# Optimization experiments

Measured on AMD Instinct MI355X. Metric: run time of the kernel, lower is better.

Reference implementation:

```python
import jax, jax.numpy as jnp
import numpy as np

NUM_HEADS = 6
HEAD_SIZE = 64
N_EMBD = 384


def setup_inputs() -> dict:
    key = jax.random.key(0)
    k1, k2, k3 = jax.random.split(key, 3)
    B, T, C = 256, 256, N_EMBD
    x = jax.random.normal(k1, (B, T, C), dtype=jnp.float32)
    # torch Linear(n_embd, 3*n_embd, bias=False): y = x @ W.T; store transposed for x @ W
    W_qkv = jax.random.normal(k2, (C, 3 * C), dtype=jnp.float32) * (1.0 / np.sqrt(C))
    W_proj = jax.random.normal(k3, (C, C), dtype=jnp.float32) * (1.0 / np.sqrt(C))
    b_proj = jnp.zeros((C,), dtype=jnp.float32)
    return {"x": x, "W_qkv": W_qkv, "W_proj": W_proj, "b_proj": b_proj}


def reference(x, W_qkv, W_proj, b_proj):
    B, T, C = x.shape
    H, D = NUM_HEADS, HEAD_SIZE
    qkv = x @ W_qkv                                  # [B, T, 3C]
    q, k, v = jnp.split(qkv, 3, axis=-1)
    # [B, T, C] -> [B, H, T, D]
    q = q.reshape(B, T, H, D).transpose(0, 2, 1, 3)
    k = k.reshape(B, T, H, D).transpose(0, 2, 1, 3)
    v = v.reshape(B, T, H, D).transpose(0, 2, 1, 3)
    att = jnp.einsum("bhtd,bhsd->bhts", q, k) / np.sqrt(D).astype(jnp.float32)
    causal = jnp.tril(jnp.ones((T, T), dtype=bool))  # tril buffer
    att = jnp.where(causal[None, None], att, -jnp.inf)
    att = jax.nn.softmax(att, axis=-1)
    # dropout layers are identity in eval mode
    out = jnp.einsum("bhts,bhsd->bhtd", att, v)      # [B, H, T, D]
    out = out.transpose(0, 2, 1, 3).reshape(B, T, C)
    return out @ W_proj.T @ jnp.eye(C, dtype=out.dtype) if False else out @ W_proj + b_proj
```

## Files before the change

### kernel.cpp

```cpp
#include <hip/hip_runtime.h>
#include <hip/hip_bf16.h>
#include <stdint.h>

typedef __hip_bfloat16 bf16;
using f32x4 = __attribute__((ext_vector_type(4))) float;
using s16x8 = __attribute__((ext_vector_type(8))) short;

#define MFMA16(A_, B_, C_) __builtin_amdgcn_mfma_f32_16x16x32_bf16((A_), (B_), (C_), 0, 0, 0)

__device__ __forceinline__ void gload16(const void* g, void* l) {
  __builtin_amdgcn_global_load_lds((const __attribute__((address_space(1))) void*)g,
                                   (__attribute__((address_space(3))) void*)l, 16, 0, 0);
}

__global__ __launch_bounds__(256) void detect_kernel(const void* __restrict__ x,
                                                     int* __restrict__ flag) {
  __shared__ int cnt;
  if (threadIdx.x == 0) cnt = 0;
  __syncthreads();
  const uint32_t* w = (const uint32_t*)x;
  int local = 0;
#pragma unroll
  for (int i = 0; i < 8; ++i) {
    uint32_t v = w[threadIdx.x * 8 + i];
    uint32_t e = (v >> 7) & 0xFF;
    if (e >= 110 && e <= 135) local++;
  }
  atomicAdd(&cnt, local);
  __syncthreads();
  if (threadIdx.x == 0) *flag = (cnt < 1024) ? 1 : 0;
}

__global__ __launch_bounds__(256) void convert_kernel(const void* __restrict__ x,
                                                      bf16* __restrict__ xb,
                                                      size_t elem_off,
                                                      const int* __restrict__ flag) {
  size_t i = ((size_t)blockIdx.x * 256 + threadIdx.x) * 8;
  if (*flag) {
    const float* xf = (const float*)x + elem_off + i;
    float4 a = ((const float4*)xf)[0];
    float4 b = ((const float4*)xf)[1];
    union { bf16 h[8]; uint4 u; } o;
    o.h[0] = __float2bfloat16(a.x); o.h[1] = __float2bfloat16(a.y);
    o.h[2] = __float2bfloat16(a.z); o.h[3] = __float2bfloat16(a.w);
    o.h[4] = __float2bfloat16(b.x); o.h[5] = __float2bfloat16(b.y);
    o.h[6] = __float2bfloat16(b.z); o.h[7] = __float2bfloat16(b.w);
    *(uint4*)(&xb[i]) = o.u;
  } else {
    *(uint4*)(&xb[i]) = *(const uint4*)((const bf16*)x + elem_off + i);
  }
}

__global__ __launch_bounds__(256) void transpose_kernel(const void* __restrict__ W,
                                                        bf16* __restrict__ Wt,
                                                        int K, int N,
                                                        const int* __restrict__ flag) {
  int idx = blockIdx.x * 256 + threadIdx.x;
  if (idx >= K * N) return;
  int n = idx / K;
  int k = idx - n * K;
  if (*flag)
    Wt[idx] = __float2bfloat16(((const float*)W)[k * N + n]);
  else
    Wt[idx] = ((const bf16*)W)[k * N + n];
}

template <int MODE>
__global__ __launch_bounds__(256) void gemm_kernel(
    const bf16* __restrict__ A, const bf16* __restrict__ Bt,
    bf16* __restrict__ qb, bf16* __restrict__ kb, bf16* __restrict__ vb,
    void* __restrict__ outp, const void* __restrict__ bias,
    int r_off, const int* __restrict__ flag) {
  constexpr int K = 384;
  __shared__ bf16 Ash[2][128 * 32];
  __shared__ bf16 Bsh[2][128 * 32];
  const int tid = threadIdx.x;
  const int lane = tid & 63;
  const int wave = tid >> 6;
  const int wm = wave & 1, wn = wave >> 1;
  const int l15 = lane & 15, quad = lane >> 4;

  const int nlin = gridDim.x * gridDim.y;
  const int orig = blockIdx.y * gridDim.x + blockIdx.x;
  const int xcd = orig & 7;
  const int q8 = nlin >> 3, r8 = nlin & 7;
  const int lin = (xcd < r8 ? xcd * (q8 + 1) : r8 * (q8 + 1) + (xcd - r8) * q8) + (orig >> 3);
  const int bx = lin % gridDim.x;
  const int by = lin / gridDim.x;
  const int n0 = bx * 128, m0 = by * 128;

  const int rl = lane >> 2;
  const int slot = lane & 3;
  const int sc = (slot - (lane >> 3)) & 3;
  const size_t lane_goff = (size_t)rl * K + sc * 8;

  const int arow0 = wave * 32;
  const bf16* Ag0 = A + (size_t)(m0 + arow0) * K + lane_goff;
  const bf16* Ag1 = Ag0 + (size_t)16 * K;
  const bf16* Bg0 = Bt + (size_t)(n0 + arow0) * K + lane_goff;
  const bf16* Bg1 = Bg0 + (size_t)16 * K;

  const int fc = ((quad + (l15 >> 1)) & 3) * 8;

  const f32x4 z4 = {0.f, 0.f, 0.f, 0.f};
  f32x4 acc[4][4];
#pragma unroll
  for (int i = 0; i < 4; ++i)
#pragma unroll
    for (int j = 0; j < 4; ++j) acc[i][j] = z4;

  auto stage = [&](int buf, int k0) {
    gload16(Ag0 + k0, &Ash[buf][arow0 * 32]);
    gload16(Ag1 + k0, &Ash[buf][(arow0 + 16) * 32]);
    gload16(Bg0 + k0, &Bsh[buf][arow0 * 32]);
    gload16(Bg1 + k0, &Bsh[buf][(arow0 + 16) * 32]);
  };

  stage(0, 0);
  __syncthreads();
  int cur = 0;
  for (int kt = 0; kt < 12; ++kt) {
    if (kt < 11) stage(cur ^ 1, (kt + 1) * 32);
    s16x8 af[4], bfr[4];
#pragma unroll
    for (int i = 0; i < 4; ++i) {
      af[i] = *(const s16x8*)(&Ash[cur][(wm * 64 + i * 16 + l15) * 32 + fc]);
      bfr[i] = *(const s16x8*)(&Bsh[cur][(wn * 64 + i * 16 + l15) * 32 + fc]);
    }
#pragma unroll
    for (int i = 0; i < 4; ++i)
#pragma unroll
      for (int j = 0; j < 4; ++j) acc[i][j] = MFMA16(af[i], bfr[j], acc[i][j]);
    __syncthreads();
    cur ^= 1;
  }

  const int mbase = m0 + wm * 64;
  const int nbase = n0 + wn * 64;
  if (MODE == 0) {
    const int sel = bx / 3;
    bf16* dst = (sel == 0) ? qb : ((sel == 1) ? kb : vb);
#pragma unroll
    for (int i = 0; i < 4; ++i) {
#pragma unroll
      for (int j = 0; j < 4; ++j) {
        int n_g = nbase + j * 16 + l15;
        int c = n_g - sel * 384;
        int h = c >> 6, d = c & 63;
#pragma unroll
        for (int r = 0; r < 4; ++r) {
          int m_loc = mbase + i * 16 + quad * 4 + r;
          int b = m_loc >> 8, t = m_loc & 255;
          bf16 bv = __float2bfloat16(acc[i][j][r]);
          int bh = b * 6 + h;
          if (sel < 2) {
            dst[(size_t)bh * 16384 + t * 64 + d] = bv;
          } else {
            int rr = t & 31;
            int pos = (((rr & 15) >> 2) << 3) | (rr & 3) | ((rr >> 4) << 2);
            int tt = (t & ~31) | pos;
            dst[(size_t)bh * 16384 + d * 256 + tt] = bv;
          }
        }
      }
    }
  } else {
    const int f32io = *flag;
#pragma unroll
    for (int i = 0; i < 4; ++i) {
#pragma unroll
      for (int j = 0; j < 4; ++j) {
        int n_g = nbase + j * 16 + l15;
        float bsv = f32io ? ((const float*)bias)[n_g]
                          : __bfloat162float(((const bf16*)bias)[n_g]);
#pragma unroll
        for (int r = 0; r < 4; ++r) {
          int m_loc = mbase + i * 16 + quad * 4 + r;
          size_t o = (size_t)(r_off + m_loc) * 384 + n_g;
          float val = acc[i][j][r] + bsv;
          if (f32io)
            ((float*)outp)[o] = val;
          else
            ((bf16*)outp)[o] = __float2bfloat16(val);
        }
      }
    }
  }
}

__global__ __launch_bounds__(256, 3) void attn_kernel(const bf16* __restrict__ Q,
                                                      const bf16* __restrict__ Kb,
                                                      const bf16* __restrict__ Vt,
                                                      bf16* __restrict__ attn_out) {
  const int tid = threadIdx.x;
  const int lane = tid & 63;
  const int wave = tid >> 6;
  const int l15 = lane & 15, quad = lane >> 4;
  const int nblk = gridDim.x;
  int blk = blockIdx.x;
  if ((nblk & 7) == 0)
    blk = (blockIdx.x & 7) * (nblk >> 3) + (blockIdx.x >> 3);
  const int p = blk & 1;
  const int bh = blk >> 1;
  const int jA = p * 4 + wave;
  const int jB = 15 - jA;
  const size_t base = (size_t)bh * 16384;
  const int q0A = jA * 16, q0B = jB * 16;

  s16x8 qA0 = *(const s16x8*)(&Q[base + (q0A + l15) * 64 + quad * 8]);
  s16x8 qA1 = *(const s16x8*)(&Q[base + (q0A + l15) * 64 + 32 + quad * 8]);
  s16x8 qB0 = *(const s16x8*)(&Q[base + (q0B + l15) * 64 + quad * 8]);
  s16x8 qB1 = *(const s16x8*)(&Q[base + (q0B + l15) * 64 + 32 + quad * 8]);

  const int ktA = (jA + 2) >> 1;
  const int ktB = (jB + 2) >> 1;
  const int tqA = q0A + l15, tqB = q0B + l15;
  const f32x4 z4 = {0.f, 0.f, 0.f, 0.f};

  const bf16* Kp = Kb + base + (size_t)l15 * 64 + quad * 8;
  const bf16* Vp = Vt + base + (size_t)l15 * 256 + quad * 8;

  typedef union { s16x8 v; uint32_t w[4]; } pf_t;

  s16x8 kf[3][4];
  s16x8 vf[2][4];
#pragma unroll
  for (int i = 0; i < 4; ++i) {
    kf[0][i] = *(const s16x8*)(Kp + (size_t)((i >> 1) * 16) * 64 + (i & 1) * 32);
    kf[1][i] = *(const s16x8*)(Kp + (size_t)(32 + (i >> 1) * 16) * 64 + (i & 1) * 32);
  }
#pragma unroll
  for (int dt = 0; dt < 4; ++dt) vf[0][dt] = *(const s16x8*)(Vp + (size_t)dt * 4096);

  f32x4 ofA[4], ofB[4];
#pragma unroll
  for (int dt = 0; dt < 4; ++dt) { ofA[dt] = z4; ofB[dt] = z4; }
  float rsA = 0.f, rsB = 0.f;

#pragma unroll
  for (int t = 0; t < 8; ++t) {
    if (t < ktB) {
      if (t + 2 < ktB) {
        const bf16* Kn = Kp + (size_t)(t + 2) * 32 * 64;
#pragma unroll
        for (int i = 0; i < 4; ++i)
          kf[(t + 2) % 3][i] = *(const s16x8*)(Kn + (size_t)((i >> 1) * 16) * 64 + (i & 1) * 32);
      }
      if (t + 1 < ktB) {
#pragma unroll
        for (int dt = 0; dt < 4; ++dt)
          vf[(t + 1) & 1][dt] = *(const s16x8*)(Vp + (size_t)dt * 4096 + (t + 1) * 32);
      }
      pf_t pfB;
#pragma unroll
      for (int hf = 0; hf < 2; ++hf) {
        const int nt = 2 * t + hf;
        if (nt <= jB) {
          f32x4 s = MFMA16(kf[t % 3][hf * 2 + 0], qB0, z4);
          s = MFMA16(kf[t % 3][hf * 2 + 1], qB1, s);
          const int tk0 = nt * 16 + quad * 4;
          float p0 = (tk0 + 0 <= tqB) ? __expf(s[0] * 0.125f) : 0.f;
          float p1 = (tk0 + 1 <= tqB) ? __expf(s[1] * 0.125f) : 0.f;
          float p2 = (tk0 + 2 <= tqB) ? __expf(s[2] * 0.125f) : 0.f;
          float p3 = (tk0 + 3 <= tqB) ? __expf(s[3] * 0.125f) : 0.f;
          rsB += (p0 + p1) + (p2 + p3);
          union { bf16 hh[2]; uint32_t u; } w0, w1;
          w0.hh[0] = __float2bfloat16(p0); w0.hh[1] = __float2bfloat16(p1);
          w1.hh[0] = __float2bfloat16(p2); w1.hh[1] = __float2bfloat16(p3);
          pfB.w[hf * 2 + 0] = w0.u;
          pfB.w[hf * 2 + 1] = w1.u;
        } else {
          pfB.w[hf * 2 + 0] = 0u;
          pfB.w[hf * 2 + 1] = 0u;
        }
      }
      if (t < ktA) {
        pf_t pfA;
#pragma unroll
        for (int hf = 0; hf < 2; ++hf) {
          const int nt = 2 * t + hf;
          if (nt <= jA) {
            f32x4 s = MFMA16(kf[t % 3][hf * 2 + 0], qA0, z4);
            s = MFMA16(kf[t % 3][hf * 2 + 1], qA1, s);
            const int tk0 = nt * 16 + quad * 4;
            float p0 = (tk0 + 0 <= tqA) ? __expf(s[0] * 0.125f) : 0.f;
            float p1 = (tk0 + 1 <= tqA) ? __expf(s[1] * 0.125f) : 0.f;
            float p2 = (tk0 + 2 <= tqA) ? __expf(s[2] * 0.125f) : 0.f;
            float p3 = (tk0 + 3 <= tqA) ? __expf(s[3] * 0.125f) : 0.f;
            rsA += (p0 + p1) + (p2 + p3);
            union { bf16 hh[2]; uint32_t u; } w0, w1;
            w0.hh[0] = __float2bfloat16(p0); w0.hh[1] = __float2bfloat16(p1);
            w1.hh[0] = __float2bfloat16(p2); w1.hh[1] = __float2bfloat16(p3);
            pfA.w[hf * 2 + 0] = w0.u;
            pfA.w[hf * 2 + 1] = w1.u;
          } else {
            pfA.w[hf * 2 + 0] = 0u;
            pfA.w[hf * 2 + 1] = 0u;
          }
        }
#pragma unroll
        for (int dt = 0; dt < 4; ++dt) ofA[dt] = MFMA16(vf[t & 1][dt], pfA.v, ofA[dt]);
      }
#pragma unroll
      for (int dt = 0; dt < 4; ++dt) ofB[dt] = MFMA16(vf[t & 1][dt], pfB.v, ofB[dt]);
    }
  }

  rsA += __shfl_xor(rsA, 16);
  rsA += __shfl_xor(rsA, 32);
  rsB += __shfl_xor(rsB, 16);
  rsB += __shfl_xor(rsB, 32);
  const float invA = 1.0f / rsA;
  const float invB = 1.0f / rsB;

  const int b = bh / 6;
  const int h = bh - b * 6;
  const size_t orowA = (size_t)(b * 256 + q0A + l15) * 384 + h * 64;
  const size_t orowB = (size_t)(b * 256 + q0B + l15) * 384 + h * 64;
#pragma unroll
  for (int dt = 0; dt < 4; ++dt) {
    union { bf16 h4[4]; uint2 u; } oa, ob;
#pragma unroll
    for (int r = 0; r < 4; ++r) {
      oa.h4[r] = __float2bfloat16(ofA[dt][r] * invA);
      ob.h4[r] = __float2bfloat16(ofB[dt][r] * invB);
    }
    *(uint2*)(&attn_out[orowA + dt * 16 + quad * 4]) = oa.u;
    *(uint2*)(&attn_out[orowB + dt * 16 + quad * 4]) = ob.u;
  }
}

extern "C" void kernel_launch(void* const* d_in, const int* in_sizes, int n_in,
                              void* d_out, int out_size, void* d_ws, size_t ws_size,
                              hipStream_t stream) {
  const void* x = d_in[0];
  const void* Wqkv = d_in[1];
  const void* Wproj = d_in[2];
  const void* bproj = d_in[3];

  char* ws = (char*)d_ws;
  int* flag = (int*)ws;                ws += 256;
  bf16* Wt_qkv = (bf16*)ws;            ws += (size_t)1152 * 384 * 2;
  bf16* Wt_proj = (bf16*)ws;           ws += (size_t)384 * 384 * 2;

  const size_t per_batch = (size_t)5 * 98304 * 2;
  size_t used = (size_t)(ws - (char*)d_ws);
  size_t remain = (ws_size > used) ? (ws_size - used) : 0;
  int NB = (int)(remain / per_batch);
  if (NB > 256) NB = 256;
  if (NB < 1) NB = 1;

  bf16* xb_buf = (bf16*)ws;
  bf16* q_buf = xb_buf + (size_t)NB * 98304;
  bf16* k_buf = q_buf + (size_t)NB * 98304;
  bf16* vt_buf = k_buf + (size_t)NB * 98304;
  bf16* attn_buf = vt_buf + (size_t)NB * 98304;

  detect_kernel<<<1, 256, 0, stream>>>(x, flag);
  transpose_kernel<<<(384 * 1152 + 255) / 256, 256, 0, stream>>>(Wqkv, Wt_qkv, 384, 1152, flag);
  transpose_kernel<<<(384 * 384 + 255) / 256, 256, 0, stream>>>(Wproj, Wt_proj, 384, 384, flag);

  for (int b0 = 0; b0 < 256; b0 += NB) {
    int nb = (256 - b0 < NB) ? (256 - b0) : NB;
    int r_off = b0 * 256;
    convert_kernel<<<nb * 48, 256, 0, stream>>>(x, xb_buf, (size_t)r_off * 384, flag);
    gemm_kernel<0><<<dim3(9, 2 * nb), 256, 0, stream>>>(
        xb_buf, Wt_qkv, q_buf, k_buf, vt_buf, nullptr, nullptr, 0, flag);
    attn_kernel<<<nb * 12, 256, 0, stream>>>(q_buf, k_buf, vt_buf, attn_buf);
    gemm_kernel<1><<<dim3(3, 2 * nb), 256, 0, stream>>>(
        attn_buf, Wt_proj, nullptr, nullptr, nullptr, d_out, bproj, r_off, flag);
  }
}
```

Measured before the change: 436.8 us.

## Enlarge GEMM tile to 256x128 with each wave owning 64 rows

The GEMM block tile grows from 128x128 to 256x128. Each of the four waves now computes a 64x128 slice, with 4x8 MFMA accumulators, and reads all eight B fragments from LDS. The goal is to cut LDS and global traffic per FLOP, since B fragments are shared across a wave's row tiles, and to halve the grid. The cost is more accumulator registers (launch bounds set to 2 waves per SIMD), twice the LDS for A, and fewer blocks, which may hurt occupancy and load balance.

```diff
diff --git a/kernel.cpp b/kernel.cpp
--- a/kernel.cpp
+++ b/kernel.cpp
@@ -66,18 +66,17 @@
 }
 
 template <int MODE>
-__global__ __launch_bounds__(256) void gemm_kernel(
+__global__ __launch_bounds__(256, 2) void gemm_kernel(
     const bf16* __restrict__ A, const bf16* __restrict__ Bt,
     bf16* __restrict__ qb, bf16* __restrict__ kb, bf16* __restrict__ vb,
     void* __restrict__ outp, const void* __restrict__ bias,
     int r_off, const int* __restrict__ flag) {
   constexpr int K = 384;
-  __shared__ bf16 Ash[2][128 * 32];
+  __shared__ bf16 Ash[2][256 * 32];
   __shared__ bf16 Bsh[2][128 * 32];
   const int tid = threadIdx.x;
   const int lane = tid & 63;
   const int wave = tid >> 6;
-  const int wm = wave & 1, wn = wave >> 1;
   const int l15 = lane & 15, quad = lane >> 4;
 
   const int nlin = gridDim.x * gridDim.y;
@@ -87,69 +86,65 @@
   const int lin = (xcd < r8 ? xcd * (q8 + 1) : r8 * (q8 + 1) + (xcd - r8) * q8) + (orig >> 3);
   const int bx = lin % gridDim.x;
   const int by = lin / gridDim.x;
-  const int n0 = bx * 128, m0 = by * 128;
+  const int n0 = bx * 128, m0 = by * 256;
 
   const int rl = lane >> 2;
   const int slot = lane & 3;
   const int sc = (slot - (lane >> 3)) & 3;
-  const size_t lane_goff = (size_t)rl * K + sc * 8;
-
-  const int arow0 = wave * 32;
-  const bf16* Ag0 = A + (size_t)(m0 + arow0) * K + lane_goff;
-  const bf16* Ag1 = Ag0 + (size_t)16 * K;
-  const bf16* Bg0 = Bt + (size_t)(n0 + arow0) * K + lane_goff;
-  const bf16* Bg1 = Bg0 + (size_t)16 * K;
+
+  const bf16* Ag = A + (size_t)(m0 + wave * 16 + rl) * K + sc * 8;
+  const bf16* Bg = Bt + (size_t)(n0 + wave * 16 + rl) * K + sc * 8;
+
+  auto stage = [&](int buf, int k0) {
+#pragma unroll
+    for (int qd = 0; qd < 4; ++qd)
+      gload16(Ag + (size_t)qd * 64 * K + k0, &Ash[buf][(qd * 64 + wave * 16) * 32]);
+#pragma unroll
+    for (int h = 0; h < 2; ++h)
+      gload16(Bg + (size_t)h * 64 * K + k0, &Bsh[buf][(h * 64 + wave * 16) * 32]);
+  };
 
   const int fc = ((quad + (l15 >> 1)) & 3) * 8;
-
   const f32x4 z4 = {0.f, 0.f, 0.f, 0.f};
-  f32x4 acc[4][4];
+  f32x4 acc[4][8];
 #pragma unroll
   for (int i = 0; i < 4; ++i)
 #pragma unroll
-    for (int j = 0; j < 4; ++j) acc[i][j] = z4;
-
-  auto stage = [&](int buf, int k0) {
-    gload16(Ag0 + k0, &Ash[buf][arow0 * 32]);
-    gload16(Ag1 + k0, &Ash[buf][(arow0 + 16) * 32]);
-    gload16(Bg0 + k0, &Bsh[buf][arow0 * 32]);
-    gload16(Bg1 + k0, &Bsh[buf][(arow0 + 16) * 32]);
-  };
+    for (int j = 0; j < 8; ++j) acc[i][j] = z4;
 
   stage(0, 0);
   __syncthreads();
   int cur = 0;
   for (int kt = 0; kt < 12; ++kt) {
     if (kt < 11) stage(cur ^ 1, (kt + 1) * 32);
-    s16x8 af[4], bfr[4];
-#pragma unroll
-    for (int i = 0; i < 4; ++i) {
-      af[i] = *(const s16x8*)(&Ash[cur][(wm * 64 + i * 16 + l15) * 32 + fc]);
-      bfr[i] = *(const s16x8*)(&Bsh[cur][(wn * 64 + i * 16 + l15) * 32 + fc]);
-    }
+    s16x8 af[4], bfr[8];
 #pragma unroll
     for (int i = 0; i < 4; ++i)
-#pragma unroll
-      for (int j = 0; j < 4; ++j) acc[i][j] = MFMA16(af[i], bfr[j], acc[i][j]);
+      af[i] = *(const s16x8*)(&Ash[cur][(wave * 64 + i * 16 + l15) * 32 + fc]);
+#pragma unroll
+    for (int j = 0; j < 8; ++j)
+      bfr[j] = *(const s16x8*)(&Bsh[cur][(j * 16 + l15) * 32 + fc]);
+#pragma unroll
+    for (int i = 0; i < 4; ++i)
+#pragma unroll
+      for (int j = 0; j < 8; ++j) acc[i][j] = MFMA16(af[i], bfr[j], acc[i][j]);
     __syncthreads();
     cur ^= 1;
   }
 
-  const int mbase = m0 + wm * 64;
-  const int nbase = n0 + wn * 64;
   if (MODE == 0) {
     const int sel = bx / 3;
     bf16* dst = (sel == 0) ? qb : ((sel == 1) ? kb : vb);
 #pragma unroll
-    for (int i = 0; i < 4; ++i) {
-#pragma unroll
-      for (int j = 0; j < 4; ++j) {
-        int n_g = nbase + j * 16 + l15;
-        int c = n_g - sel * 384;
-        int h = c >> 6, d = c & 63;
+    for (int j = 0; j < 8; ++j) {
+      int n_g = n0 + j * 16 + l15;
+      int c = n_g - sel * 384;
+      int h = c >> 6, d = c & 63;
+#pragma unroll
+      for (int i = 0; i < 4; ++i) {
 #pragma unroll
         for (int r = 0; r < 4; ++r) {
-          int m_loc = mbase + i * 16 + quad * 4 + r;
+          int m_loc = m0 + wave * 64 + i * 16 + quad * 4 + r;
           int b = m_loc >> 8, t = m_loc & 255;
           bf16 bv = __float2bfloat16(acc[i][j][r]);
           int bh = b * 6 + h;
@@ -167,15 +162,15 @@
   } else {
     const int f32io = *flag;
 #pragma unroll
-    for (int i = 0; i < 4; ++i) {
-#pragma unroll
-      for (int j = 0; j < 4; ++j) {
-        int n_g = nbase + j * 16 + l15;
-        float bsv = f32io ? ((const float*)bias)[n_g]
-                          : __bfloat162float(((const bf16*)bias)[n_g]);
+    for (int j = 0; j < 8; ++j) {
+      int n_g = n0 + j * 16 + l15;
+      float bsv = f32io ? ((const float*)bias)[n_g]
+                        : __bfloat162float(((const bf16*)bias)[n_g]);
+#pragma unroll
+      for (int i = 0; i < 4; ++i) {
 #pragma unroll
         for (int r = 0; r < 4; ++r) {
-          int m_loc = mbase + i * 16 + quad * 4 + r;
+          int m_loc = m0 + wave * 64 + i * 16 + quad * 4 + r;
           size_t o = (size_t)(r_off + m_loc) * 384 + n_g;
           float val = acc[i][j][r] + bsv;
           if (f32io)
@@ -364,10 +359,10 @@
     int nb = (256 - b0 < NB) ? (256 - b0) : NB;
     int r_off = b0 * 256;
     convert_kernel<<<nb * 48, 256, 0, stream>>>(x, xb_buf, (size_t)r_off * 384, flag);
-    gemm_kernel<0><<<dim3(9, 2 * nb), 256, 0, stream>>>(
+    gemm_kernel<0><<<dim3(9, nb), 256, 0, stream>>>(
         xb_buf, Wt_qkv, q_buf, k_buf, vt_buf, nullptr, nullptr, 0, flag);
     attn_kernel<<<nb * 12, 256, 0, stream>>>(q_buf, k_buf, vt_buf, attn_buf);
-    gemm_kernel<1><<<dim3(3, 2 * nb), 256, 0, stream>>>(
+    gemm_kernel<1><<<dim3(3, nb), 256, 0, stream>>>(
         attn_buf, Wt_proj, nullptr, nullptr, nullptr, d_out, bproj, r_off, flag);
   }
 }
```

Result: slower. 453.1 us (+3.7%).
